# Kernel optimization log

Measured on AMD Instinct MI355X. Metric: run time of the kernel, lower is better.

The kernel has to match this reference:

```python
import jax, jax.numpy as jnp
import numpy as np

N, D, C = 131072, 256, 1000
EPS = 1e-6


def setup_inputs() -> dict:
    key = jax.random.key(0)
    k1, k2, k3, k4 = jax.random.split(key, 4)
    feats = jax.random.normal(k1, (N, D), dtype=jnp.float32)
    pseudo_lbls = jax.random.randint(k2, (N,), 0, C)
    src_proto = jax.random.normal(k3, (C, D), dtype=jnp.float32)
    # uniform in [0.5, 1.5) to keep the Mahalanobis denominator well-conditioned
    src_proto_cov = jax.random.uniform(k4, (C, D), dtype=jnp.float32) + 0.5
    return {"feats": feats, "pseudo_lbls": pseudo_lbls,
            "src_proto": src_proto, "src_proto_cov": src_proto_cov}


def reference(feats, pseudo_lbls, src_proto, src_proto_cov):
    # Fused scatter-mean over classes (replaces the python loop over unique labels).
    num_classes, feat_dim = src_proto.shape
    counts = jax.ops.segment_sum(jnp.ones((feats.shape[0],), feats.dtype),
                                 pseudo_lbls, num_segments=num_classes)  # [C]
    sums = jax.ops.segment_sum(feats, pseudo_lbls, num_segments=num_classes)  # [C, D]
    means = sums / jnp.maximum(counts, 1.0)[:, None]                      # [C, D]
    present = counts > 0                                                  # [C]
    # GSSLoss: mean over the [n_uniq, D] elements of (mean - proto)^2 / (cov + eps)
    per_elem = (means - src_proto) ** 2 / (src_proto_cov + EPS)           # [C, D]
    per_elem = jnp.where(present[:, None], per_elem, 0.0)
    n_present = jnp.sum(present.astype(feats.dtype))
    loss = jnp.sum(per_elem) / (n_present * feat_dim)
    return loss
```

## Files before the change

### kernel.cpp

```cpp
#include <hip/hip_runtime.h>

#define EPS 1e-6f
#define CAP 512


__global__ void bucket_kernel(const int* __restrict__ lbls,
                              int* __restrict__ counts,
                              int* __restrict__ rowidx, int n) {
    int i = blockIdx.x * blockDim.x + threadIdx.x;
    if (i < n) {
        int l = lbls[i];
        int pos = atomicAdd(&counts[l], 1);
        if (pos < CAP) rowidx[(size_t)l * CAP + pos] = i;
    }
}

__global__ __launch_bounds__(256)
void fused_kernel(const float* __restrict__ feats,
                  const int* __restrict__ rowidx,
                  const int* __restrict__ counts,
                  const float* __restrict__ proto,
                  const float* __restrict__ cov,
                  float* __restrict__ loss_acc,
                  float* __restrict__ npres_acc,
                  int* __restrict__ done,
                  float* __restrict__ out, int c_total, int d) {
    int c    = blockIdx.x;
    int t    = threadIdx.x;
    int wave = t >> 6;
    int col4 = t & 63;
    int stride4 = d >> 2;

    int cnt = counts[c];
    int m   = cnt > CAP ? CAP : cnt;

    __shared__ int sidx[CAP];
    for (int i = t; i < m; i += 256)
        sidx[i] = rowidx[(size_t)c * CAP + i];
    __syncthreads();

    const float4* f4 = (const float4*)feats;
    float4 acc = make_float4(0.f, 0.f, 0.f, 0.f);

    int i = wave;
    for (; i + 28 < m; i += 32) {
        int r0 = sidx[i];
        int r1 = sidx[i + 4];
        int r2 = sidx[i + 8];
        int r3 = sidx[i + 12];
        int r4 = sidx[i + 16];
        int r5 = sidx[i + 20];
        int r6 = sidx[i + 24];
        int r7 = sidx[i + 28];
        float4 v0 = f4[(size_t)r0 * stride4 + col4];
        float4 v1 = f4[(size_t)r1 * stride4 + col4];
        float4 v2 = f4[(size_t)r2 * stride4 + col4];
        float4 v3 = f4[(size_t)r3 * stride4 + col4];
        float4 v4 = f4[(size_t)r4 * stride4 + col4];
        float4 v5 = f4[(size_t)r5 * stride4 + col4];
        float4 v6 = f4[(size_t)r6 * stride4 + col4];
        float4 v7 = f4[(size_t)r7 * stride4 + col4];
        acc.x += ((v0.x + v1.x) + (v2.x + v3.x)) + ((v4.x + v5.x) + (v6.x + v7.x));
        acc.y += ((v0.y + v1.y) + (v2.y + v3.y)) + ((v4.y + v5.y) + (v6.y + v7.y));
        acc.z += ((v0.z + v1.z) + (v2.z + v3.z)) + ((v4.z + v5.z) + (v6.z + v7.z));
        acc.w += ((v0.w + v1.w) + (v2.w + v3.w)) + ((v4.w + v5.w) + (v6.w + v7.w));
    }
    for (; i < m; i += 4) {
        int r0 = sidx[i];
        float4 v0 = f4[(size_t)r0 * stride4 + col4];
        acc.x += v0.x; acc.y += v0.y; acc.z += v0.z; acc.w += v0.w;
    }

    __shared__ float4 sacc[256];
    sacc[t] = acc;
    __syncthreads();

    if (t < 64) {
        float4 a0 = sacc[t], a1 = sacc[t + 64], a2 = sacc[t + 128], a3 = sacc[t + 192];
        float4 r;
        r.x = (a0.x + a1.x) + (a2.x + a3.x);
        r.y = (a0.y + a1.y) + (a2.y + a3.y);
        r.z = (a0.z + a1.z) + (a2.z + a3.z);
        r.w = (a0.w + a1.w) + (a2.w + a3.w);

        float present = (cnt > 0) ? 1.0f : 0.0f;
        float inv = 1.0f / fmaxf((float)cnt, 1.0f);
        float4 p4 = ((const float4*)proto)[(size_t)c * stride4 + t];
        float4 c4 = ((const float4*)cov)[(size_t)c * stride4 + t];
        float dx = r.x * inv - p4.x;
        float dy = r.y * inv - p4.y;
        float dz = r.z * inv - p4.z;
        float dw = r.w * inv - p4.w;
        float pe = present * ((dx * dx / (c4.x + EPS) + dy * dy / (c4.y + EPS)) +
                              (dz * dz / (c4.z + EPS) + dw * dw / (c4.w + EPS)));

        for (int off = 32; off > 0; off >>= 1)
            pe += __shfl_down(pe, off, 64);

        if (t == 0) {
            atomicAdd(loss_acc, pe);
            atomicAdd(npres_acc, present);
            __threadfence();
            int prev = atomicAdd(done, 1);
            if (prev == c_total - 1) {
                float L = atomicAdd(loss_acc, 0.0f);
                float P = atomicAdd(npres_acc, 0.0f);
                out[0] = L / (P * (float)d);
            }
        }
    }
}

extern "C" void kernel_launch(void* const* d_in, const int* in_sizes, int n_in,
                              void* d_out, int out_size, void* d_ws, size_t ws_size,
                              hipStream_t stream) {
    const float* feats = (const float*)d_in[0];
    const int*   lbls  = (const int*)d_in[1];
    const float* proto = (const float*)d_in[2];
    const float* cov   = (const float*)d_in[3];

    int n_rows = in_sizes[1];
    int d      = in_sizes[0] / n_rows;
    int c      = in_sizes[2] / d;

    int*   counts    = (int*)d_ws;
    float* loss_acc  = (float*)d_ws + c;
    float* npres_acc = loss_acc + 1;
    int*   done      = (int*)d_ws + c + 2;
    int*   rowidx    = (int*)d_ws + c + 3;

    hipMemsetAsync(d_ws, 0, ((size_t)c + 3) * sizeof(int), stream);

    int nb = (n_rows + 255) / 256;
    bucket_kernel<<<nb, 256, 0, stream>>>(lbls, counts, rowidx, n_rows);
    fused_kernel<<<c, 256, 0, stream>>>(feats, rowidx, counts, proto, cov,
                                        loss_acc, npres_acc, done,
                                        (float*)d_out, c, d);
}
```

Measured before the change: 274.1 us.

## Stage gathered feature rows into LDS via async global_load_lds double buffering

Replaces the direct register float4 gather with asynchronous global-to-LDS loads (global_load_lds, 16 bytes per lane). Each wave owns a double-buffered staging area of 8 rows, prefetching the next batch while it accumulates the current one, with explicit vmcnt waits between them. The aim is to keep more memory requests in flight and hide gather latency. In exchange it uses about 64KB of LDS per block, which lowers occupancy, and it relies on hand-written waitcnt counts being correct.

```diff
diff --git a/kernel.cpp b/kernel.cpp
--- a/kernel.cpp
+++ b/kernel.cpp
@@ -2,6 +2,8 @@
 
 #define EPS 1e-6f
 #define CAP 512
+#define NW 4
+#define RB 8
 
 
 __global__ void bucket_kernel(const int* __restrict__ lbls,
@@ -15,68 +17,88 @@
     }
 }
 
+__device__ __forceinline__ void dma16(const float* g, float* l) {
+    __builtin_amdgcn_global_load_lds(
+        (const __attribute__((address_space(1))) unsigned int*)g,
+        (__attribute__((address_space(3))) unsigned int*)l, 16, 0, 0);
+}
+
 __global__ __launch_bounds__(256)
-void fused_kernel(const float* __restrict__ feats,
-                  const int* __restrict__ rowidx,
-                  const int* __restrict__ counts,
-                  const float* __restrict__ proto,
-                  const float* __restrict__ cov,
-                  float* __restrict__ loss_acc,
-                  float* __restrict__ npres_acc,
-                  int* __restrict__ done,
-                  float* __restrict__ out, int c_total, int d) {
+void gather_kernel(const float* __restrict__ feats,
+                   const int* __restrict__ rowidx,
+                   const int* __restrict__ counts,
+                   const float* __restrict__ proto,
+                   const float* __restrict__ cov,
+                   float* __restrict__ loss_acc,
+                   float* __restrict__ npres_acc,
+                   int* __restrict__ done,
+                   float* __restrict__ out, int c_total, int d) {
     int c    = blockIdx.x;
     int t    = threadIdx.x;
-    int wave = t >> 6;
-    int col4 = t & 63;
-    int stride4 = d >> 2;
+    int w    = t >> 6;
+    int lane = t & 63;
+
+    __shared__ int   sidx[CAP];
+    __shared__ float stage[NW][2][RB][256];
+    __shared__ float4 sacc[NW][64];
 
     int cnt = counts[c];
-    int m   = cnt > CAP ? CAP : cnt;
+    int m = cnt > CAP ? CAP : cnt;
 
-    __shared__ int sidx[CAP];
-    for (int i = t; i < m; i += 256)
-        sidx[i] = rowidx[(size_t)c * CAP + i];
+    for (int i = t; i < m; i += 256) sidx[i] = rowidx[(size_t)c * CAP + i];
     __syncthreads();
 
-    const float4* f4 = (const float4*)feats;
     float4 acc = make_float4(0.f, 0.f, 0.f, 0.f);
 
-    int i = wave;
-    for (; i + 28 < m; i += 32) {
-        int r0 = sidx[i];
-        int r1 = sidx[i + 4];
-        int r2 = sidx[i + 8];
-        int r3 = sidx[i + 12];
-        int r4 = sidx[i + 16];
-        int r5 = sidx[i + 20];
-        int r6 = sidx[i + 24];
-        int r7 = sidx[i + 28];
-        float4 v0 = f4[(size_t)r0 * stride4 + col4];
-        float4 v1 = f4[(size_t)r1 * stride4 + col4];
-        float4 v2 = f4[(size_t)r2 * stride4 + col4];
-        float4 v3 = f4[(size_t)r3 * stride4 + col4];
-        float4 v4 = f4[(size_t)r4 * stride4 + col4];
-        float4 v5 = f4[(size_t)r5 * stride4 + col4];
-        float4 v6 = f4[(size_t)r6 * stride4 + col4];
-        float4 v7 = f4[(size_t)r7 * stride4 + col4];
-        acc.x += ((v0.x + v1.x) + (v2.x + v3.x)) + ((v4.x + v5.x) + (v6.x + v7.x));
-        acc.y += ((v0.y + v1.y) + (v2.y + v3.y)) + ((v4.y + v5.y) + (v6.y + v7.y));
-        acc.z += ((v0.z + v1.z) + (v2.z + v3.z)) + ((v4.z + v5.z) + (v6.z + v7.z));
-        acc.w += ((v0.w + v1.w) + (v2.w + v3.w)) + ((v4.w + v5.w) + (v6.w + v7.w));
-    }
-    for (; i < m; i += 4) {
-        int r0 = sidx[i];
-        float4 v0 = f4[(size_t)r0 * stride4 + col4];
-        acc.x += v0.x; acc.y += v0.y; acc.z += v0.z; acc.w += v0.w;
+    if (m > 0) {
+        int nsb = (m + (NW * RB) - 1) / (NW * RB);
+
+        auto issue = [&](int sb, int buf) {
+            int r0 = sb * (NW * RB) + w * RB;
+            #pragma unroll
+            for (int k = 0; k < RB; ++k) {
+                int ri = r0 + k;
+                if (ri < m) {
+                    int row = sidx[ri];
+                    dma16(feats + (size_t)row * d + lane * 4,
+                          &stage[w][buf][k][0]);
+                }
+            }
+        };
+
+        issue(0, 0);
+        for (int sb = 0; sb < nsb; ++sb) {
+            int buf = sb & 1;
+            if (sb + 1 < nsb) {
+                int r0n = (sb + 1) * (NW * RB) + w * RB;
+                issue(sb + 1, buf ^ 1);
+                if (r0n + RB <= m) {
+                    asm volatile("s_waitcnt vmcnt(8)" ::: "memory");
+                } else {
+                    asm volatile("s_waitcnt vmcnt(0)" ::: "memory");
+                }
+            } else {
+                asm volatile("s_waitcnt vmcnt(0)" ::: "memory");
+            }
+            __builtin_amdgcn_sched_barrier(0);
+
+            int r0 = sb * (NW * RB) + w * RB;
+            #pragma unroll
+            for (int k = 0; k < RB; ++k) {
+                if (r0 + k < m) {
+                    float4 v = *(const float4*)&stage[w][buf][k][lane * 4];
+                    acc.x += v.x; acc.y += v.y; acc.z += v.z; acc.w += v.w;
+                }
+            }
+        }
     }
 
-    __shared__ float4 sacc[256];
-    sacc[t] = acc;
+    sacc[w][lane] = acc;
     __syncthreads();
 
-    if (t < 64) {
-        float4 a0 = sacc[t], a1 = sacc[t + 64], a2 = sacc[t + 128], a3 = sacc[t + 192];
+    if (w == 0) {
+        float4 a0 = sacc[0][lane], a1 = sacc[1][lane];
+        float4 a2 = sacc[2][lane], a3 = sacc[3][lane];
         float4 r;
         r.x = (a0.x + a1.x) + (a2.x + a3.x);
         r.y = (a0.y + a1.y) + (a2.y + a3.y);
@@ -85,8 +107,9 @@
 
         float present = (cnt > 0) ? 1.0f : 0.0f;
         float inv = 1.0f / fmaxf((float)cnt, 1.0f);
-        float4 p4 = ((const float4*)proto)[(size_t)c * stride4 + t];
-        float4 c4 = ((const float4*)cov)[(size_t)c * stride4 + t];
+        int d4 = d >> 2;
+        float4 p4 = ((const float4*)proto)[(size_t)c * d4 + lane];
+        float4 c4 = ((const float4*)cov)[(size_t)c * d4 + lane];
         float dx = r.x * inv - p4.x;
         float dy = r.y * inv - p4.y;
         float dz = r.z * inv - p4.z;
@@ -97,7 +120,7 @@
         for (int off = 32; off > 0; off >>= 1)
             pe += __shfl_down(pe, off, 64);
 
-        if (t == 0) {
+        if (lane == 0) {
             atomicAdd(loss_acc, pe);
             atomicAdd(npres_acc, present);
             __threadfence();
@@ -133,7 +156,7 @@
 
     int nb = (n_rows + 255) / 256;
     bucket_kernel<<<nb, 256, 0, stream>>>(lbls, counts, rowidx, n_rows);
-    fused_kernel<<<c, 256, 0, stream>>>(feats, rowidx, counts, proto, cov,
-                                        loss_acc, npres_acc, done,
-                                        (float*)d_out, c, d);
+    gather_kernel<<<c, 256, 0, stream>>>(feats, rowidx, counts, proto, cov,
+                                         loss_acc, npres_acc, done,
+                                         (float*)d_out, c, d);
 }
```

New measurement: 265.3 us. -3.2%, faster.
